# Optimization experiments

Measured on AMD Instinct MI355X. Metric: run time of the kernel, lower is better.

## Reference

```python
import jax, jax.numpy as jnp
import numpy as np

B, S, D, H = 2, 2048, 1024, 16
HS = D // H  # head size 64
EPS = 1e-5


def setup_inputs() -> dict:
    key = jax.random.key(0)
    ks = jax.random.split(key, 12)
    s = lambda fan_in: 1.0 / np.sqrt(fan_in)
    return {
        "x": jax.random.normal(ks[0], (B, S, D), dtype=jnp.float32),
        # per-head QKV weights, math orientation [H, D, HS] (x @ W)
        "wq": jax.random.normal(ks[1], (H, D, HS), dtype=jnp.float32) * s(D),
        "wk": jax.random.normal(ks[2], (H, D, HS), dtype=jnp.float32) * s(D),
        "wv": jax.random.normal(ks[3], (H, D, HS), dtype=jnp.float32) * s(D),
        "wproj": jax.random.normal(ks[4], (D, D), dtype=jnp.float32) * s(D),
        "bproj": jnp.zeros((D,), dtype=jnp.float32),
        "w1": jax.random.normal(ks[5], (D, 4 * D), dtype=jnp.float32) * s(D),
        "b1": jnp.zeros((4 * D,), dtype=jnp.float32),
        "w2": jax.random.normal(ks[6], (4 * D, D), dtype=jnp.float32) * s(4 * D),
        "b2": jnp.zeros((D,), dtype=jnp.float32),
        "ln1_g": jnp.ones((D,), dtype=jnp.float32),
        "ln1_b": jnp.zeros((D,), dtype=jnp.float32),
        "ln2_g": jnp.ones((D,), dtype=jnp.float32),
        "ln2_b": jnp.zeros((D,), dtype=jnp.float32),
    }


def _layernorm(x, g, b):
    mu = jnp.mean(x, axis=-1, keepdims=True)
    var = jnp.mean(jnp.square(x - mu), axis=-1, keepdims=True)
    return (x - mu) * jax.lax.rsqrt(var + EPS) * g + b


def reference(x, wq, wk, wv, wproj, bproj, w1, b1, w2, b2, ln1_g, ln1_b, ln2_g, ln2_b):
    Bq, T, C = x.shape
    xn = _layernorm(x, ln1_g, ln1_b)
    # per-head projections, batched over heads
    q = jnp.einsum('btd,hdk->bhtk', xn, wq)
    k = jnp.einsum('btd,hdk->bhtk', xn, wk)
    v = jnp.einsum('btd,hdk->bhtk', xn, wv)
    scale = k.shape[-1] ** (-0.5)
    scores = jnp.einsum('bhtk,bhsk->bhts', q, k) * scale  # [B,H,T,T]
    causal = jnp.tril(jnp.ones((T, T), dtype=bool))
    scores = jnp.where(causal, scores, -jnp.inf)
    att = jax.nn.softmax(scores, axis=-1)
    out = jnp.einsum('bhts,bhsk->bhtk', att, v)  # [B,H,T,HS]
    out = out.transpose(0, 2, 1, 3).reshape(Bq, T, C)  # concat heads
    attn_out = out @ wproj + bproj
    h = x + attn_out
    hn = _layernorm(h, ln2_g, ln2_b)
    ff = jax.nn.relu(hn @ w1 + b1) @ w2 + b2
    return h + ff
```

## Files before the change

kernel.cpp:

```cpp
#include <hip/hip_runtime.h>


typedef __bf16 bf16_t;
typedef __attribute__((ext_vector_type(8))) __bf16 bf16x8;
typedef __attribute__((ext_vector_type(4))) __bf16 bf16x4;
typedef __attribute__((ext_vector_type(4))) float f32x4;

__device__ __forceinline__ f32x4 mfma16(bf16x8 a, bf16x8 b, f32x4 c) {
  return __builtin_amdgcn_mfma_f32_16x16x32_bf16(a, b, c, 0, 0, 0);
}

__device__ __forceinline__ void gll16(const void* g, void* l) {
  __builtin_amdgcn_global_load_lds(
      (const __attribute__((address_space(1))) void*)g,
      (__attribute__((address_space(3))) void*)l, 16, 0, 0);
}

__global__ __launch_bounds__(256) void ln_kernel(
    const float* __restrict__ x, const float* __restrict__ g,
    const float* __restrict__ be, bf16_t* __restrict__ out) {
  const int row = blockIdx.x;
  const int tid = threadIdx.x;
  const float4 v = *(reinterpret_cast<const float4*>(x + (size_t)row * 1024) + tid);
  float s1 = v.x + v.y + v.z + v.w;
  float s2 = v.x * v.x + v.y * v.y + v.z * v.z + v.w * v.w;
#pragma unroll
  for (int off = 1; off < 64; off <<= 1) {
    s1 += __shfl_xor(s1, off);
    s2 += __shfl_xor(s2, off);
  }
  __shared__ float red[8];
  const int l = tid & 63, w = tid >> 6;
  if (l == 0) { red[w] = s1; red[w + 4] = s2; }
  __syncthreads();
  s1 = red[0] + red[1] + red[2] + red[3];
  s2 = red[4] + red[5] + red[6] + red[7];
  const float mu = s1 * (1.f / 1024.f);
  const float var = s2 * (1.f / 1024.f) - mu * mu;
  const float rstd = rsqrtf(var + 1e-5f);
  const float4 gg = *(reinterpret_cast<const float4*>(g) + tid);
  const float4 bb = *(reinterpret_cast<const float4*>(be) + tid);
  bf16x4 o;
  o[0] = (bf16_t)((v.x - mu) * rstd * gg.x + bb.x);
  o[1] = (bf16_t)((v.y - mu) * rstd * gg.y + bb.y);
  o[2] = (bf16_t)((v.z - mu) * rstd * gg.z + bb.z);
  o[3] = (bf16_t)((v.w - mu) * rstd * gg.w + bb.w);
  *(reinterpret_cast<bf16x4*>(out + (size_t)row * 1024) + tid) = o;
}

__global__ __launch_bounds__(256) void ln2_red_kernel(
    const float* __restrict__ p, const float* __restrict__ bp,
    const float* __restrict__ x, const float* __restrict__ g,
    const float* __restrict__ be, float* __restrict__ hb,
    bf16_t* __restrict__ out) {
  const size_t PM = (size_t)4096 * 1024;
  const int row = blockIdx.x;
  const int tid = threadIdx.x;
  const size_t ro = (size_t)row * 1024;
  float4 v = *(reinterpret_cast<const float4*>(p + ro) + tid);
  const float4 v1 = *(reinterpret_cast<const float4*>(p + PM + ro) + tid);
  const float4 vb = *(reinterpret_cast<const float4*>(bp) + tid);
  const float4 vx = *(reinterpret_cast<const float4*>(x + ro) + tid);
  v.x += v1.x + vb.x + vx.x; v.y += v1.y + vb.y + vx.y;
  v.z += v1.z + vb.z + vx.z; v.w += v1.w + vb.w + vx.w;
  *(reinterpret_cast<float4*>(hb + ro) + tid) = v;
  float s1 = v.x + v.y + v.z + v.w;
  float s2 = v.x * v.x + v.y * v.y + v.z * v.z + v.w * v.w;
#pragma unroll
  for (int off = 1; off < 64; off <<= 1) {
    s1 += __shfl_xor(s1, off);
    s2 += __shfl_xor(s2, off);
  }
  __shared__ float red[8];
  const int l = tid & 63, w = tid >> 6;
  if (l == 0) { red[w] = s1; red[w + 4] = s2; }
  __syncthreads();
  s1 = red[0] + red[1] + red[2] + red[3];
  s2 = red[4] + red[5] + red[6] + red[7];
  const float mu = s1 * (1.f / 1024.f);
  const float var = s2 * (1.f / 1024.f) - mu * mu;
  const float rstd = rsqrtf(var + 1e-5f);
  const float4 gg = *(reinterpret_cast<const float4*>(g) + tid);
  const float4 bb = *(reinterpret_cast<const float4*>(be) + tid);
  bf16x4 o;
  o[0] = (bf16_t)((v.x - mu) * rstd * gg.x + bb.x);
  o[1] = (bf16_t)((v.y - mu) * rstd * gg.y + bb.y);
  o[2] = (bf16_t)((v.z - mu) * rstd * gg.z + bb.z);
  o[3] = (bf16_t)((v.w - mu) * rstd * gg.w + bb.w);
  *(reinterpret_cast<bf16x4*>(out + ro) + tid) = o;
}

__global__ __launch_bounds__(256) void red4_kernel(
    const float* __restrict__ p, const float* __restrict__ b2,
    const float* __restrict__ hb, float* __restrict__ out) {
  const size_t PM = (size_t)4096 * 1024;
  const int row = blockIdx.x;
  const int tid = threadIdx.x;
  const size_t ro = (size_t)row * 1024;
  float4 v = *(reinterpret_cast<const float4*>(p + ro) + tid);
#pragma unroll
  for (int s = 1; s < 4; s++) {
    const float4 vs = *(reinterpret_cast<const float4*>(p + s * PM + ro) + tid);
    v.x += vs.x; v.y += vs.y; v.z += vs.z; v.w += vs.w;
  }
  const float4 vb = *(reinterpret_cast<const float4*>(b2) + tid);
  const float4 vh = *(reinterpret_cast<const float4*>(hb + ro) + tid);
  v.x += vb.x + vh.x; v.y += vb.y + vh.y;
  v.z += vb.z + vh.z; v.w += vb.w + vh.w;
  *(reinterpret_cast<float4*>(out + ro) + tid) = v;
}

__global__ __launch_bounds__(256) void transpose_cvt(
    const float* __restrict__ in, bf16_t* __restrict__ out, int R, int C) {
  __shared__ float t[32][33];
  const int bz = blockIdx.z;
  in += (size_t)bz * R * C;
  out += (size_t)bz * R * C;
  const int c0 = blockIdx.x * 32, r0 = blockIdx.y * 32;
  const int tx = threadIdx.x, ty = threadIdx.y;
#pragma unroll
  for (int i = 0; i < 4; i++)
    t[ty + i * 8][tx] = in[(size_t)(r0 + ty + i * 8) * C + c0 + tx];
  __syncthreads();
#pragma unroll
  for (int i = 0; i < 4; i++)
    out[(size_t)(c0 + ty + i * 8) * R + r0 + tx] = (bf16_t)t[tx][ty + i * 8];
}

template <int MODE>
__global__ __launch_bounds__(256) void gemm_bt(
    const bf16_t* __restrict__ A, const bf16_t* __restrict__ BT,
    const float* __restrict__ bias, const float* __restrict__ resid,
    void* __restrict__ out0, void* __restrict__ out1, int M, int N, int K) {
  __shared__ __align__(16) bf16_t Al[128 * 32];
  __shared__ __align__(16) bf16_t Bl[128 * 32];
  const int tid = threadIdx.x;
  const int l = tid & 63, w = tid >> 6;
  const int wr = w >> 1, wc = w & 1;
  const int lr = l & 15, lg = l >> 4;
  const int gx = gridDim.x;
  const int nwg = gx * gridDim.y;
  int flat = blockIdx.y * gx + blockIdx.x;
  flat = (flat & 7) * (nwg >> 3) + (flat >> 3);
  const int bm = (flat / gx) * 128, bn = (flat % gx) * 128;

  int k0 = 0, nK = K >> 5;
  if constexpr (MODE == 3) {
    const int chunk = K / gridDim.z;
    k0 = blockIdx.z * chunk;
    nK = chunk >> 5;
  }

  f32x4 acc[4][4];
#pragma unroll
  for (int i = 0; i < 4; i++)
#pragma unroll
    for (int j = 0; j < 4; j++) acc[i][j] = (f32x4)(0.f);

  const char* Ag = (const char*)(A + (size_t)bm * K + k0);
  const char* Bg = (const char*)(BT + (size_t)bn * K + k0);
  const size_t rowb = (size_t)K * 2;

  for (int kt = 0; kt < nK; ++kt) {
#pragma unroll
    for (int i = 0; i < 2; i++) {
      const int s = i * 256 + tid;
      const size_t go = (size_t)(s >> 2) * rowb + (size_t)(kt * 64 + (s & 3) * 16);
      gll16(Ag + go, (char*)Al + (i * 256 + w * 64) * 16);
      gll16(Bg + go, (char*)Bl + (i * 256 + w * 64) * 16);
    }
    __syncthreads();
    bf16x8 af[4], bfr[4];
#pragma unroll
    for (int mi = 0; mi < 4; mi++)
      af[mi] = *reinterpret_cast<const bf16x8*>(Al + (wr * 64 + mi * 16 + lr) * 32 + lg * 8);
#pragma unroll
    for (int ni = 0; ni < 4; ni++)
      bfr[ni] = *reinterpret_cast<const bf16x8*>(Bl + (wc * 64 + ni * 16 + lr) * 32 + lg * 8);
#pragma unroll
    for (int mi = 0; mi < 4; mi++)
#pragma unroll
      for (int ni = 0; ni < 4; ni++)
        acc[mi][ni] = mfma16(af[mi], bfr[ni], acc[mi][ni]);
    __syncthreads();
  }

#pragma unroll
  for (int mi = 0; mi < 4; mi++) {
    const int r = bm + wr * 64 + mi * 16 + lg * 4;
#pragma unroll
    for (int ni = 0; ni < 4; ni++) {
      const int c = bn + wc * 64 + ni * 16 + lr;
      f32x4 v = acc[mi][ni];
      if constexpr (MODE == 1) {
        const float bb = bias[c];
        float* o = (float*)out0;
#pragma unroll
        for (int j = 0; j < 4; j++)
          o[(size_t)(r + j) * N + c] = v[j] + bb + resid[(size_t)(r + j) * N + c];
      } else if constexpr (MODE == 2) {
        const float bb = bias[c];
        bf16_t* o = (bf16_t*)out0;
#pragma unroll
        for (int j = 0; j < 4; j++)
          o[(size_t)(r + j) * N + c] = (bf16_t)fmaxf(v[j] + bb, 0.f);
      } else if constexpr (MODE == 3) {
        float* o = (float*)out0 + (size_t)blockIdx.z * M * N;
#pragma unroll
        for (int j = 0; j < 4; j++)
          o[(size_t)(r + j) * N + c] = v[j];
      } else {
        if (c < 2048) {
          bf16_t* o = (bf16_t*)out0;
#pragma unroll
          for (int j = 0; j < 4; j++)
            o[(size_t)(r + j) * 2048 + c] = (bf16_t)v[j];
        } else {
          const int nn = c - 2048;
          const int bI = r >> 11, tl = r & 2047;
          bf16x4 pk;
#pragma unroll
          for (int j = 0; j < 4; j++) pk[j] = (bf16_t)v[j];
          *reinterpret_cast<bf16x4*>((bf16_t*)out1 +
              ((size_t)(bI * 1024 + nn)) * 2048 + tl) = pk;
        }
      }
    }
  }
}

__device__ __forceinline__ void attn_tile(
    const bf16_t* __restrict__ kl, const bf16_t* __restrict__ vl,
    bf16_t* __restrict__ plw, const bf16x8* qf, f32x4* oacc,
    float* mrow, float* lrow, const int lr, const int lg,
    const int rbase, const int cbase, const bool diag) {
  f32x4 sc4[4];
#pragma unroll
  for (int ct = 0; ct < 4; ct++) sc4[ct] = (f32x4)(0.f);
#pragma unroll
  for (int ct = 0; ct < 4; ct++)
#pragma unroll
    for (int kc = 0; kc < 2; kc++) {
      bf16x8 kf = *reinterpret_cast<const bf16x8*>(
          &kl[(ct * 16 + lr) * 72 + kc * 32 + lg * 8]);
      sc4[ct] = mfma16(qf[kc], kf, sc4[ct]);
    }
#pragma unroll
  for (int ct = 0; ct < 4; ct++)
#pragma unroll
    for (int j = 0; j < 4; j++) {
      float sv = sc4[ct][j] * 0.125f;
      if (diag && (cbase + ct * 16 + lr > rbase + j)) sv = -1e30f;
      sc4[ct][j] = sv;
    }
  float rmax[4];
#pragma unroll
  for (int j = 0; j < 4; j++)
    rmax[j] = fmaxf(fmaxf(sc4[0][j], sc4[1][j]), fmaxf(sc4[2][j], sc4[3][j]));
#pragma unroll
  for (int off = 1; off < 16; off <<= 1)
#pragma unroll
    for (int j = 0; j < 4; j++) rmax[j] = fmaxf(rmax[j], __shfl_xor(rmax[j], off));
  float fac[4];
#pragma unroll
  for (int j = 0; j < 4; j++) {
    const float mn = fmaxf(mrow[j], rmax[j]);
    fac[j] = __expf(mrow[j] - mn);
    mrow[j] = mn;
  }
  float rsum[4] = {0.f, 0.f, 0.f, 0.f};
#pragma unroll
  for (int ct = 0; ct < 4; ct++)
#pragma unroll
    for (int j = 0; j < 4; j++) {
      const float pv = __expf(sc4[ct][j] - mrow[j]);
      sc4[ct][j] = pv;
      rsum[j] += pv;
    }
#pragma unroll
  for (int off = 1; off < 16; off <<= 1)
#pragma unroll
    for (int j = 0; j < 4; j++) rsum[j] += __shfl_xor(rsum[j], off);
#pragma unroll
  for (int j = 0; j < 4; j++) lrow[j] = lrow[j] * fac[j] + rsum[j];
#pragma unroll
  for (int ht = 0; ht < 4; ht++)
#pragma unroll
    for (int j = 0; j < 4; j++) oacc[ht][j] *= fac[j];
#pragma unroll
  for (int ct = 0; ct < 4; ct++)
#pragma unroll
    for (int j = 0; j < 4; j++)
      plw[(lg * 4 + j) * 72 + ct * 16 + lr] = (bf16_t)sc4[ct][j];
  bf16x8 pf[2];
#pragma unroll
  for (int sc = 0; sc < 2; sc++)
    pf[sc] = *reinterpret_cast<const bf16x8*>(&plw[lr * 72 + sc * 32 + lg * 8]);
#pragma unroll
  for (int ht = 0; ht < 4; ht++)
#pragma unroll
    for (int sc = 0; sc < 2; sc++) {
      bf16x8 vf = *reinterpret_cast<const bf16x8*>(
          &vl[(ht * 16 + lr) * 72 + sc * 32 + lg * 8]);
      oacc[ht] = mfma16(pf[sc], vf, oacc[ht]);
    }
}

__global__ __launch_bounds__(256) void attn_kernel(
    const bf16_t* __restrict__ qk, const bf16_t* __restrict__ vT,
    bf16_t* __restrict__ ac) {
  const int f = blockIdx.x;
  const int bh = (f & 7) + 8 * ((f >> 3) & 3);
  const int p = f >> 5;
  const int qlo = p, qhi = 31 - p;
  const int b = bh >> 4, h = bh & 15;
  const int tid = threadIdx.x;
  const int l = tid & 63, w = tid >> 6;
  const int lr = l & 15, lg = l >> 4;

  __shared__ __align__(16) bf16_t kl[64 * 72];
  __shared__ __align__(16) bf16_t vl[64 * 72];
  __shared__ __align__(16) bf16_t pl[4][16 * 72];
  bf16_t* plw = pl[w];

  const bf16_t* qb = qk + ((size_t)(b * 2048 + w * 16 + lr)) * 2048 + h * 64;
  bf16x8 qfl[2], qfh[2];
#pragma unroll
  for (int kc = 0; kc < 2; kc++) {
    qfl[kc] = *(const bf16x8*)(qb + (size_t)qlo * 64 * 2048 + kc * 32 + lg * 8);
    qfh[kc] = *(const bf16x8*)(qb + (size_t)qhi * 64 * 2048 + kc * 32 + lg * 8);
  }

  f32x4 oaccl[4], oacch[4];
  float ml[4], llo[4], mh[4], lhi[4];
#pragma unroll
  for (int i = 0; i < 4; i++) { oaccl[i] = (f32x4)(0.f); oacch[i] = (f32x4)(0.f); }
#pragma unroll
  for (int j = 0; j < 4; j++) { ml[j] = -1e30f; llo[j] = 0.f; mh[j] = -1e30f; lhi[j] = 0.f; }

  const int rlo = qlo * 64 + w * 16 + lg * 4;
  const int rhi = qhi * 64 + w * 16 + lg * 4;

  const int r0 = tid >> 3, c0 = (tid & 7) * 8;
  const bf16_t* kg = qk + ((size_t)(b * 2048)) * 2048 + 1024 + h * 64;
  const bf16_t* vg = vT + ((size_t)(bh * 64)) * 2048;

  bf16x8 kreg[2], vreg[2];
#pragma unroll
  for (int i = 0; i < 2; i++) {
    const int r = r0 + i * 32;
    kreg[i] = *(const bf16x8*)(kg + (size_t)r * 2048 + c0);
    vreg[i] = *(const bf16x8*)(vg + (size_t)r * 2048 + c0);
  }

  const int nst = qhi + 1;
  for (int st = 0; st < nst; ++st) {
    __syncthreads();
#pragma unroll
    for (int i = 0; i < 2; i++) {
      const int r = r0 + i * 32;
      *(bf16x8*)(&kl[r * 72 + c0]) = kreg[i];
      *(bf16x8*)(&vl[r * 72 + c0]) = vreg[i];
    }
    __syncthreads();
    if (st + 1 < nst) {
#pragma unroll
      for (int i = 0; i < 2; i++) {
        const int r = r0 + i * 32;
        kreg[i] = *(const bf16x8*)(kg + (size_t)((st + 1) * 64 + r) * 2048 + c0);
        vreg[i] = *(const bf16x8*)(vg + (size_t)r * 2048 + (st + 1) * 64 + c0);
      }
    }
    attn_tile(kl, vl, plw, qfh, oacch, mh, lhi, lr, lg, rhi, st * 64, st == qhi);
    if (st <= qlo)
      attn_tile(kl, vl, plw, qfl, oaccl, ml, llo, lr, lg, rlo, st * 64, st == qlo);
  }

#pragma unroll
  for (int ht = 0; ht < 4; ht++)
#pragma unroll
    for (int j = 0; j < 4; j++) {
      const size_t tl = (size_t)(b * 2048 + rlo + j);
      ac[tl * 1024 + h * 64 + ht * 16 + lr] = (bf16_t)(oaccl[ht][j] / llo[j]);
      const size_t th = (size_t)(b * 2048 + rhi + j);
      ac[th * 1024 + h * 64 + ht * 16 + lr] = (bf16_t)(oacch[ht][j] / lhi[j]);
    }
}

extern "C" void kernel_launch(void* const* d_in, const int* in_sizes, int n_in,
                              void* d_out, int out_size, void* d_ws, size_t ws_size,
                              hipStream_t stream) {
  const float* x     = (const float*)d_in[0];
  const float* wq    = (const float*)d_in[1];
  const float* wk    = (const float*)d_in[2];
  const float* wv    = (const float*)d_in[3];
  const float* wproj = (const float*)d_in[4];
  const float* bproj = (const float*)d_in[5];
  const float* w1    = (const float*)d_in[6];
  const float* b1    = (const float*)d_in[7];
  const float* w2    = (const float*)d_in[8];
  const float* b2    = (const float*)d_in[9];
  const float* ln1g  = (const float*)d_in[10];
  const float* ln1b  = (const float*)d_in[11];
  const float* ln2g  = (const float*)d_in[12];
  const float* ln2b  = (const float*)d_in[13];
  float* out = (float*)d_out;

  char* ws = (char*)d_ws;
  const size_t MB = 1 << 20;
  bf16_t* xn  = (bf16_t*)(ws + 0);
  bf16_t* wT  = (bf16_t*)(ws + 8 * MB);
  float*  hbuf= (float*)(ws + 16 * MB);
  bf16_t* qkb = (bf16_t*)(ws + 32 * MB);
  bf16_t* vTb = (bf16_t*)(ws + 48 * MB);
  bf16_t* acb = (bf16_t*)(ws + 56 * MB);
  bf16_t* ffa = (bf16_t*)(ws + 32 * MB);
  float*  part= (float*)(ws + 64 * MB);
  bf16_t* hn  = xn;

  const bool big = ws_size >= 128 * MB;
  dim3 tb(32, 8);

  ln_kernel<<<4096, 256, 0, stream>>>(x, ln1g, ln1b, xn);
  transpose_cvt<<<dim3(2, 32, 16), tb, 0, stream>>>(wq, wT, 1024, 64);
  transpose_cvt<<<dim3(2, 32, 16), tb, 0, stream>>>(wk, wT + 1024 * 1024, 1024, 64);
  transpose_cvt<<<dim3(2, 32, 16), tb, 0, stream>>>(wv, wT + 2048 * 1024, 1024, 64);
  gemm_bt<0><<<dim3(24, 32), 256, 0, stream>>>(xn, wT, nullptr, nullptr, qkb, vTb,
                                               4096, 3072, 1024);
  attn_kernel<<<512, 256, 0, stream>>>(qkb, vTb, acb);
  transpose_cvt<<<dim3(32, 32, 1), tb, 0, stream>>>(wproj, wT, 1024, 1024);
  if (big) {
    gemm_bt<3><<<dim3(8, 32, 2), 256, 0, stream>>>(acb, wT, nullptr, nullptr,
                                                   part, nullptr, 4096, 1024, 1024);
    ln2_red_kernel<<<4096, 256, 0, stream>>>(part, bproj, x, ln2g, ln2b, hbuf, hn);
  } else {
    gemm_bt<1><<<dim3(8, 32), 256, 0, stream>>>(acb, wT, bproj, x, hbuf, nullptr,
                                                4096, 1024, 1024);
    ln_kernel<<<4096, 256, 0, stream>>>(hbuf, ln2g, ln2b, hn);
  }
  transpose_cvt<<<dim3(128, 32, 1), tb, 0, stream>>>(w1, wT, 1024, 4096);
  gemm_bt<2><<<dim3(32, 32), 256, 0, stream>>>(hn, wT, b1, nullptr, ffa, nullptr,
                                               4096, 4096, 1024);
  transpose_cvt<<<dim3(32, 128, 1), tb, 0, stream>>>(w2, wT, 4096, 1024);
  if (big) {
    gemm_bt<3><<<dim3(8, 32, 4), 256, 0, stream>>>(ffa, wT, nullptr, nullptr,
                                                   part, nullptr, 4096, 1024, 4096);
    red4_kernel<<<4096, 256, 0, stream>>>(part, b2, hbuf, out);
  } else {
    gemm_bt<1><<<dim3(8, 32), 256, 0, stream>>>(ffa, wT, b2, hbuf, out, nullptr,
                                                4096, 1024, 4096);
  }
}
```

Before: 413.0 us.

## Split attention KV range across two blocks and merge partials in a combine kernel

```diff
diff --git a/kernel.cpp b/kernel.cpp
--- a/kernel.cpp
+++ b/kernel.cpp
@@ -306,13 +306,20 @@
     }
 }
 
+template <int SPLIT>
 __global__ __launch_bounds__(256) void attn_kernel(
     const bf16_t* __restrict__ qk, const bf16_t* __restrict__ vT,
-    bf16_t* __restrict__ ac) {
+    bf16_t* __restrict__ ac, float* __restrict__ po,
+    float* __restrict__ mlb) {
   const int f = blockIdx.x;
   const int bh = (f & 7) + 8 * ((f >> 3) & 3);
-  const int p = f >> 5;
+  const int p = (f >> 5) & 15;
+  const int half = SPLIT ? (f >> 9) : 0;
   const int qlo = p, qhi = 31 - p;
+  const int nst = qhi + 1;
+  const int kcut = SPLIT ? (p >= 7 ? 8 : 16 - p) : nst;
+  const int st0 = half ? kcut : 0;
+  const int st1 = half ? nst : kcut;
   const int b = bh >> 4, h = bh & 15;
   const int tid = threadIdx.x;
   const int l = tid & 63, w = tid >> 6;
@@ -349,12 +356,11 @@
 #pragma unroll
   for (int i = 0; i < 2; i++) {
     const int r = r0 + i * 32;
-    kreg[i] = *(const bf16x8*)(kg + (size_t)r * 2048 + c0);
-    vreg[i] = *(const bf16x8*)(vg + (size_t)r * 2048 + c0);
-  }
-
-  const int nst = qhi + 1;
-  for (int st = 0; st < nst; ++st) {
+    kreg[i] = *(const bf16x8*)(kg + (size_t)(st0 * 64 + r) * 2048 + c0);
+    vreg[i] = *(const bf16x8*)(vg + (size_t)r * 2048 + st0 * 64 + c0);
+  }
+
+  for (int st = st0; st < st1; ++st) {
     __syncthreads();
 #pragma unroll
     for (int i = 0; i < 2; i++) {
@@ -363,7 +369,7 @@
       *(bf16x8*)(&vl[r * 72 + c0]) = vreg[i];
     }
     __syncthreads();
-    if (st + 1 < nst) {
+    if (st + 1 < st1) {
 #pragma unroll
       for (int i = 0; i < 2; i++) {
         const int r = r0 + i * 32;
@@ -376,15 +382,59 @@
       attn_tile(kl, vl, plw, qfl, oaccl, ml, llo, lr, lg, rlo, st * 64, st == qlo);
   }
 
-#pragma unroll
-  for (int ht = 0; ht < 4; ht++)
-#pragma unroll
-    for (int j = 0; j < 4; j++) {
-      const size_t tl = (size_t)(b * 2048 + rlo + j);
-      ac[tl * 1024 + h * 64 + ht * 16 + lr] = (bf16_t)(oaccl[ht][j] / llo[j]);
-      const size_t th = (size_t)(b * 2048 + rhi + j);
-      ac[th * 1024 + h * 64 + ht * 16 + lr] = (bf16_t)(oacch[ht][j] / lhi[j]);
-    }
+  if constexpr (SPLIT == 0) {
+#pragma unroll
+    for (int ht = 0; ht < 4; ht++)
+#pragma unroll
+      for (int j = 0; j < 4; j++) {
+        const size_t tl = (size_t)(b * 2048 + rlo + j);
+        ac[tl * 1024 + h * 64 + ht * 16 + lr] = (bf16_t)(oaccl[ht][j] / llo[j]);
+        const size_t th = (size_t)(b * 2048 + rhi + j);
+        ac[th * 1024 + h * 64 + ht * 16 + lr] = (bf16_t)(oacch[ht][j] / lhi[j]);
+      }
+  } else {
+    float* poh = po + (size_t)half * 65536 * 64;
+    const size_t base = (size_t)bh * 2048;
+#pragma unroll
+    for (int ht = 0; ht < 4; ht++)
+#pragma unroll
+      for (int j = 0; j < 4; j++) {
+        poh[(base + rlo + j) * 64 + ht * 16 + lr] = oaccl[ht][j];
+        poh[(base + rhi + j) * 64 + ht * 16 + lr] = oacch[ht][j];
+      }
+    if (lr == 0) {
+      float2* mlh = (float2*)mlb + (size_t)half * 65536 + base;
+#pragma unroll
+      for (int j = 0; j < 4; j++) {
+        mlh[rlo + j] = make_float2(ml[j], llo[j]);
+        mlh[rhi + j] = make_float2(mh[j], lhi[j]);
+      }
+    }
+  }
+}
+
+__global__ __launch_bounds__(256) void attn_combine(
+    const float* __restrict__ po, const float* __restrict__ mlb,
+    bf16_t* __restrict__ ac) {
+  const int t = threadIdx.x;
+  const int row = blockIdx.x * 16 + (t >> 4);
+  const int hs4 = (t & 15) * 4;
+  const size_t HALF = (size_t)65536 * 64;
+  const float2 ml0 = ((const float2*)mlb)[row];
+  const float2 ml1 = ((const float2*)mlb)[65536 + row];
+  const float m = fmaxf(ml0.x, ml1.x);
+  const float w0 = __expf(ml0.x - m), w1 = __expf(ml1.x - m);
+  const float inv = 1.f / (ml0.y * w0 + ml1.y * w1);
+  const float4 o0 = *(const float4*)(po + (size_t)row * 64 + hs4);
+  const float4 o1 = *(const float4*)(po + HALF + (size_t)row * 64 + hs4);
+  const int bh = row >> 11, qr = row & 2047;
+  const int b = bh >> 4, h = bh & 15;
+  bf16x4 o;
+  o[0] = (bf16_t)((o0.x * w0 + o1.x * w1) * inv);
+  o[1] = (bf16_t)((o0.y * w0 + o1.y * w1) * inv);
+  o[2] = (bf16_t)((o0.z * w0 + o1.z * w1) * inv);
+  o[3] = (bf16_t)((o0.w * w0 + o1.w * w1) * inv);
+  *(bf16x4*)(ac + ((size_t)(b * 2048 + qr)) * 1024 + h * 64 + hs4) = o;
 }
 
 extern "C" void kernel_launch(void* const* d_in, const int* in_sizes, int n_in,
@@ -416,6 +466,8 @@
   bf16_t* acb = (bf16_t*)(ws + 56 * MB);
   bf16_t* ffa = (bf16_t*)(ws + 32 * MB);
   float*  part= (float*)(ws + 64 * MB);
+  float*  po  = (float*)(ws + 64 * MB);
+  float*  mlb = (float*)(ws + 96 * MB);
   bf16_t* hn  = xn;
 
   const bool big = ws_size >= 128 * MB;
@@ -427,7 +479,12 @@
   transpose_cvt<<<dim3(2, 32, 16), tb, 0, stream>>>(wv, wT + 2048 * 1024, 1024, 64);
   gemm_bt<0><<<dim3(24, 32), 256, 0, stream>>>(xn, wT, nullptr, nullptr, qkb, vTb,
                                                4096, 3072, 1024);
-  attn_kernel<<<512, 256, 0, stream>>>(qkb, vTb, acb);
+  if (big) {
+    attn_kernel<1><<<1024, 256, 0, stream>>>(qkb, vTb, acb, po, mlb);
+    attn_combine<<<4096, 256, 0, stream>>>(po, mlb, acb);
+  } else {
+    attn_kernel<0><<<512, 256, 0, stream>>>(qkb, vTb, acb, nullptr, nullptr);
+  }
   transpose_cvt<<<dim3(32, 32, 1), tb, 0, stream>>>(wproj, wT, 1024, 1024);
   if (big) {
     gemm_bt<3><<<dim3(8, 32, 2), 256, 0, stream>>>(acb, wT, nullptr, nullptr,
```

After: 424.7 us. +2.8%, slower.
